# Kernel optimization log

Measured on AMD Instinct MI355X. Metric: run time of the kernel, lower is better.

The kernel has to match this reference:

```python
import jax, jax.numpy as jnp
import numpy as np

VOCAB, X, H, C_CLS = 32000, 300, 512, 5
B, N_LEAVES = 256, 256  # complete binary trees, depth 9, 511 nodes/tree

def setup_inputs() -> dict:
    key = jax.random.key(0)
    ks = jax.random.split(key, 10)
    s = lambda k, shp, fan: jax.random.normal(k, shp, jnp.float32) * (1.0 / np.sqrt(fan))
    return {
        'wordid': jax.random.randint(ks[0], (B, N_LEAVES), 0, VOCAB),
        'emb': jax.random.normal(ks[1], (VOCAB, X), jnp.float32) * 0.1,
        'W_iou_w': s(ks[2], (3 * H, X), X),
        'W_iou_b': jnp.zeros((3 * H,), jnp.float32),
        'U_iou_w': s(ks[3], (3 * H, 2 * H), 2 * H),
        'U_iou_b': jnp.zeros((3 * H,), jnp.float32),
        'U_f_w': s(ks[4], (2 * H, 2 * H), 2 * H),
        'U_f_b': jnp.zeros((2 * H,), jnp.float32),
        'lin_w': s(ks[5], (C_CLS, H), H),
        'lin_b': jnp.zeros((C_CLS,), jnp.float32),
    }

def _cell(iou, c_f):
    i, o, u = jnp.split(iou, 3, axis=-1)
    c = jax.nn.sigmoid(i) * jnp.tanh(u) + c_f
    h = jax.nn.sigmoid(o) * jnp.tanh(c)
    return h, c

def reference(wordid, emb, W_iou_w, W_iou_b, U_iou_w, U_iou_b, U_f_w, U_f_b, lin_w, lin_b):
    b, n = wordid.shape
    # leaves: is_leaf=1 -> iou = W_iou(x), c_f = 0
    x = emb[wordid]                                   # [B, L, X]
    iou = x @ W_iou_w.T + W_iou_b                     # [B, L, 3H]
    h, c = _cell(iou, 0.0)
    hs = [h]
    # internal levels: reduce over exactly 2 children (binary TreeLSTM)
    while h.shape[1] > 1:
        m = h.shape[1] // 2
        h_cat = h.reshape(b, m, 2 * H)                # concat of 2 children
        c_pair = c.reshape(b, m, 2, H)
        f = jax.nn.sigmoid(h_cat @ U_f_w.T + U_f_b).reshape(b, m, 2, H)
        c_f = jnp.sum(f * c_pair, axis=2)             # [B, m, H]
        iou = h_cat @ U_iou_w.T + U_iou_b             # is_leaf=0 branch
        h, c = _cell(iou, c_f)
        hs.append(h)
    h_all = jnp.concatenate(hs, axis=1)               # [B, 2L-1, H], leaves-first topo order
    # dropout is identity at inference
    logits = h_all @ lin_w.T + lin_b                  # [B, 2L-1, num_classes]
    return logits
```

## Files before the change

kernel.cpp:

```cpp
#include <hip/hip_runtime.h>
#include <hip/hip_bf16.h>


typedef __bf16 bf16;
typedef bf16  bf16x8 __attribute__((ext_vector_type(8)));
typedef float f32x4  __attribute__((ext_vector_type(4)));

__device__ __forceinline__ float sigm(float x){ return 1.0f/(1.0f + __expf(-x)); }
__device__ __forceinline__ float tanh_f(float x){ return 1.0f - 2.0f/(__expf(2.0f*x)+1.0f); }

__global__ void cvt_pad_w(const float* __restrict__ src, bf16* __restrict__ dst){
  const int row = blockIdx.x, c = threadIdx.x;
  dst[row*320 + c] = (bf16)(c < 300 ? src[row*300 + c] : 0.f);
}
__global__ void cvt_emb(const float* __restrict__ src, bf16* __restrict__ dst){
  const int row = blockIdx.x, c = threadIdx.x;
  dst[row*320 + c] = (bf16)(c < 300 ? src[(size_t)row*300 + c] : 0.f);
}
__global__ void cvt_u(const float* __restrict__ Uiou, const float* __restrict__ Uf,
                      bf16* __restrict__ dst){
  const int i = blockIdx.x*256 + threadIdx.x;
  if (i < 2560*1024)
    dst[i] = (bf16)(i < 1536*1024 ? Uiou[i] : Uf[i - 1536*1024]);
}

__global__ __launch_bounds__(256, 2)
void leaf128_kernel(const int* __restrict__ wordid, const bf16* __restrict__ embp,
                    const bf16* __restrict__ Wpad, const float* __restrict__ Wb,
                    bf16* __restrict__ hcur, float* __restrict__ ccur)
{
  __shared__ bf16 lsA[128*40];
  __shared__ bf16 lsB[3][64*40];
  const int t = threadIdx.x;
  const int mrow0 = blockIdx.x*128, nblk = blockIdx.y*64;
  const int r = t>>2, kc = (t&3)*8;
  const int lane16 = t&15, quad = (t&63)>>4, w = t>>6;

  f32x4 acc[3][8];
  const f32x4 zero = {0.f,0.f,0.f,0.f};
  #pragma unroll
  for(int o=0;o<3;o++){
    #pragma unroll
    for(int rt=0;rt<8;rt++) acc[o][rt]=zero;
  }

  const int wid0 = wordid[mrow0 + r];
  const int wid1 = wordid[mrow0 + 64 + r];
  const bf16* arow0 = embp + (size_t)wid0*320;
  const bf16* arow1 = embp + (size_t)wid1*320;
  const int col = nblk + r;
  for (int k0=0;k0<320;k0+=32){
    *(bf16x8*)&lsA[r*40+kc]      = *(const bf16x8*)&arow0[k0+kc];
    *(bf16x8*)&lsA[(64+r)*40+kc] = *(const bf16x8*)&arow1[k0+kc];
    #pragma unroll
    for(int g=0;g<3;g++)
      *(bf16x8*)&lsB[g][r*40+kc] = *(const bf16x8*)&Wpad[(size_t)(g*512+col)*320 + k0+kc];
    __syncthreads();
    bf16x8 bfrag[3];
    #pragma unroll
    for(int g=0;g<3;g++) bfrag[g] = *(const bf16x8*)&lsB[g][(w*16+lane16)*40 + quad*8];
    #pragma unroll
    for(int rt=0;rt<8;rt++){
      bf16x8 a = *(const bf16x8*)&lsA[(rt*16+lane16)*40 + quad*8];
      #pragma unroll
      for(int g=0;g<3;g++)
        acc[g][rt] = __builtin_amdgcn_mfma_f32_16x16x32_bf16(a, bfrag[g], acc[g][rt], 0,0,0);
    }
    __syncthreads();
  }
  const int j = nblk + w*16 + lane16;
  const float bi=Wb[j], bo=Wb[512+j], bu=Wb[1024+j];
  #pragma unroll
  for(int rt=0;rt<8;rt++){
    #pragma unroll
    for(int reg=0;reg<4;reg++){
      const int row = mrow0 + rt*16 + quad*4 + reg;
      float iv=acc[0][rt][reg]+bi, ov=acc[1][rt][reg]+bo, uv=acc[2][rt][reg]+bu;
      float c = sigm(iv)*tanh_f(uv);
      float h = sigm(ov)*tanh_f(c);
      ccur[(size_t)row*512 + j] = c;
      hcur[(size_t)row*512 + j] = (bf16)h;
    }
  }
}

__global__ __launch_bounds__(256)
void level_kernel(const bf16* __restrict__ hprev, bf16* __restrict__ hcur,
                  const float* __restrict__ cprev, float* __restrict__ ccur,
                  const bf16* __restrict__ Uall, const float* __restrict__ Uioub,
                  const float* __restrict__ Ufb)
{
  __shared__ bf16 lsA[64*40];
  __shared__ bf16 lsB[5][64*40];
  const int t = threadIdx.x;
  const int mrow0 = blockIdx.x*64, nblk = blockIdx.y*64;
  const int r = t>>2, kc = (t&3)*8;
  const int lane16 = t&15, quad = (t&63)>>4, w = t>>6;

  f32x4 acc[5][4];
  const f32x4 zero = {0.f,0.f,0.f,0.f};
  #pragma unroll
  for(int o=0;o<5;o++){
    #pragma unroll
    for(int rt=0;rt<4;rt++) acc[o][rt]=zero;
  }

  const bf16* arow = hprev + (size_t)(mrow0 + r)*1024;
  const int col = nblk + r;
  for (int k0=0;k0<1024;k0+=32){
    *(bf16x8*)&lsA[r*40+kc] = *(const bf16x8*)&arow[k0+kc];
    #pragma unroll
    for(int g=0;g<5;g++)
      *(bf16x8*)&lsB[g][r*40+kc] = *(const bf16x8*)&Uall[(size_t)(g*512+col)*1024 + k0+kc];
    __syncthreads();
    bf16x8 bfrag[5];
    #pragma unroll
    for(int o=0;o<5;o++) bfrag[o] = *(const bf16x8*)&lsB[o][(w*16+lane16)*40 + quad*8];
    #pragma unroll
    for(int rt=0;rt<4;rt++){
      bf16x8 a = *(const bf16x8*)&lsA[(rt*16+lane16)*40 + quad*8];
      #pragma unroll
      for(int o=0;o<5;o++)
        acc[o][rt] = __builtin_amdgcn_mfma_f32_16x16x32_bf16(a, bfrag[o], acc[o][rt], 0,0,0);
    }
    __syncthreads();
  }
  const int j = nblk + w*16 + lane16;
  const float bi =Uioub[j], bo=Uioub[512+j], bu=Uioub[1024+j];
  const float bfl=Ufb[j],   bfr=Ufb[512+j];
  #pragma unroll
  for(int rt=0;rt<4;rt++){
    #pragma unroll
    for(int reg=0;reg<4;reg++){
      const int row = mrow0 + rt*16 + quad*4 + reg;
      float iv=acc[0][rt][reg]+bi, ov=acc[1][rt][reg]+bo, uv=acc[2][rt][reg]+bu;
      float fl=acc[3][rt][reg]+bfl, fr=acc[4][rt][reg]+bfr;
      float cl = cprev[((size_t)row*2  )*512 + j];
      float cr = cprev[((size_t)row*2+1)*512 + j];
      float cf = sigm(fl)*cl + sigm(fr)*cr;
      float c  = sigm(iv)*tanh_f(uv) + cf;
      float h  = sigm(ov)*tanh_f(c);
      ccur[(size_t)row*512 + j] = c;
      hcur[(size_t)row*512 + j] = (bf16)h;
    }
  }
}

__global__ __launch_bounds__(256, 2)
void level128_kernel(const bf16* __restrict__ hprev, bf16* __restrict__ hcur,
                     const float* __restrict__ cprev, float* __restrict__ ccur,
                     const bf16* __restrict__ Uall, const float* __restrict__ Uioub,
                     const float* __restrict__ Ufb)
{
  __shared__ bf16 lsA[128*40];
  __shared__ bf16 lsB[5][64*40];
  const int t = threadIdx.x;
  const int mrow0 = blockIdx.x*128, nblk = blockIdx.y*64;
  const int r = t>>2, kc = (t&3)*8;
  const int lane16 = t&15, quad = (t&63)>>4, w = t>>6;

  f32x4 acc[5][8];
  const f32x4 zero = {0.f,0.f,0.f,0.f};
  #pragma unroll
  for(int o=0;o<5;o++){
    #pragma unroll
    for(int rt=0;rt<8;rt++) acc[o][rt]=zero;
  }

  const bf16* arow0 = hprev + (size_t)(mrow0 + r)*1024;
  const bf16* arow1 = hprev + (size_t)(mrow0 + 64 + r)*1024;
  const int col = nblk + r;
  for (int k0=0;k0<1024;k0+=32){
    *(bf16x8*)&lsA[r*40+kc]      = *(const bf16x8*)&arow0[k0+kc];
    *(bf16x8*)&lsA[(64+r)*40+kc] = *(const bf16x8*)&arow1[k0+kc];
    #pragma unroll
    for(int g=0;g<5;g++)
      *(bf16x8*)&lsB[g][r*40+kc] = *(const bf16x8*)&Uall[(size_t)(g*512+col)*1024 + k0+kc];
    __syncthreads();
    bf16x8 bfrag[5];
    #pragma unroll
    for(int g=0;g<5;g++) bfrag[g] = *(const bf16x8*)&lsB[g][(w*16+lane16)*40 + quad*8];
    #pragma unroll
    for(int rt=0;rt<8;rt++){
      bf16x8 a = *(const bf16x8*)&lsA[(rt*16+lane16)*40 + quad*8];
      #pragma unroll
      for(int g=0;g<5;g++)
        acc[g][rt] = __builtin_amdgcn_mfma_f32_16x16x32_bf16(a, bfrag[g], acc[g][rt], 0,0,0);
    }
    __syncthreads();
  }
  const int j = nblk + w*16 + lane16;
  const float bi =Uioub[j], bo=Uioub[512+j], bu=Uioub[1024+j];
  const float bfl=Ufb[j],   bfr=Ufb[512+j];
  #pragma unroll
  for(int rt=0;rt<8;rt++){
    #pragma unroll
    for(int reg=0;reg<4;reg++){
      const int row = mrow0 + rt*16 + quad*4 + reg;
      float iv=acc[0][rt][reg]+bi, ov=acc[1][rt][reg]+bo, uv=acc[2][rt][reg]+bu;
      float fl=acc[3][rt][reg]+bfl, fr=acc[4][rt][reg]+bfr;
      float cl = cprev[((size_t)row*2  )*512 + j];
      float cr = cprev[((size_t)row*2+1)*512 + j];
      float cf = sigm(fl)*cl + sigm(fr)*cr;
      float c  = sigm(iv)*tanh_f(uv) + cf;
      float h  = sigm(ov)*tanh_f(c);
      ccur[(size_t)row*512 + j] = c;
      hcur[(size_t)row*512 + j] = (bf16)h;
    }
  }
}

__global__ __launch_bounds__(256)
void logits_kernel(const bf16* __restrict__ h, const float* __restrict__ linw,
                   const float* __restrict__ linb, float* __restrict__ out,
                   int rowbase, int lgm, int mask, int off){
  const int row = blockIdx.x*4 + (threadIdx.x>>6);
  const int l = threadIdx.x & 63;
  bf16x8 hv = *(const bf16x8*)(h + (size_t)row*512 + l*8);
  float hf[8];
  #pragma unroll
  for(int jj=0;jj<8;jj++) hf[jj] = (float)hv[jj];
  float s[5];
  #pragma unroll
  for(int c=0;c<5;c++){
    const f32x4 w0 = *(const f32x4*)(linw + c*512 + l*8);
    const f32x4 w1 = *(const f32x4*)(linw + c*512 + l*8 + 4);
    float a = 0.f;
    #pragma unroll
    for(int jj=0;jj<4;jj++) a += hf[jj]*w0[jj] + hf[4+jj]*w1[jj];
    s[c]=a;
  }
  #pragma unroll
  for(int o=32;o>0;o>>=1){
    #pragma unroll
    for(int c=0;c<5;c++) s[c] += __shfl_down(s[c], o, 64);
  }
  if (l==0){
    const int g = rowbase + row;
    const int node = (g>>lgm)*511 + off + (g&mask);
    #pragma unroll
    for(int c=0;c<5;c++) out[(size_t)node*5+c] = s[c] + linb[c];
  }
}

__global__ void zero_out(float* out, int n){
  int i = blockIdx.x*256 + threadIdx.x;
  if (i < n) out[i] = 0.f;
}

extern "C" void kernel_launch(void* const* d_in, const int* in_sizes, int n_in,
                              void* d_out, int out_size, void* d_ws, size_t ws_size,
                              hipStream_t stream)
{
  const int*   wordid = (const int*)d_in[0];
  const float* emb    = (const float*)d_in[1];
  const float* Wiou   = (const float*)d_in[2];
  const float* Wioub  = (const float*)d_in[3];
  const float* Uiou   = (const float*)d_in[4];
  const float* Uioub  = (const float*)d_in[5];
  const float* Uf     = (const float*)d_in[6];
  const float* Ufb    = (const float*)d_in[7];
  const float* linw   = (const float*)d_in[8];
  const float* linb   = (const float*)d_in[9];
  float* out = (float*)d_out;

  const size_t oWPD  = 0;
  const size_t oUALL = oWPD  + (size_t)1536*320*2;
  const size_t oEMB  = oUALL + (size_t)2560*1024*2;
  const size_t oH1   = oEMB  + (size_t)32000*320*2;
  const size_t oC1   = oH1   + (size_t)32768*512*2;
  const size_t oH0   = oC1   + (size_t)32768*512*4;
  size_t R0 = 0;
  {
    const size_t t2 = oH0 + (size_t)32768*512*(2+4);
    const size_t t4 = oH0 + (size_t)16384*512*(2+4);
    const size_t t8 = oH0 + (size_t) 8192*512*(2+4);
    if      (ws_size >= t2) R0 = 32768;
    else if (ws_size >= t4) R0 = 16384;
    else if (ws_size >= t8) R0 = 8192;
  }
  if (R0 == 0){
    zero_out<<<(out_size+255)/256, 256, 0, stream>>>(out, out_size);
    return;
  }

  char* ws = (char*)d_ws;
  bf16*  Wpad = (bf16*)(ws + oWPD);
  bf16*  Uall = (bf16*)(ws + oUALL);
  bf16*  embp = (bf16*)(ws + oEMB);
  bf16*  h1   = (bf16*)(ws + oH1);
  float* c1   = (float*)(ws + oC1);
  bf16*  h0   = (bf16*)(ws + oH0);
  float* c0   = (float*)(ws + oH0 + R0*1024);

  cvt_pad_w<<<1536, 320, 0, stream>>>(Wiou, Wpad);
  cvt_u<<<(2560*1024+255)/256, 256, 0, stream>>>(Uiou, Uf, Uall);
  cvt_emb<<<32000, 320, 0, stream>>>(emb, embp);

  const int offs[9] = {0,256,384,448,480,496,504,508,510};
  const int nchunk = (int)(65536 / R0);

  for (int ch = 0; ch < nchunk; ch++){
    const int* wid = wordid + (size_t)ch*R0;
    leaf128_kernel<<<dim3((int)(R0/128), 8), 256, 0, stream>>>(wid, embp, Wpad, Wioub,
                                                               h0, c0);
    logits_kernel<<<(int)(R0/4), 256, 0, stream>>>(h0, linw, linb, out,
                                                   (int)(ch*R0), 8, 255, 0);
    bf16*  h1c = h1 + (size_t)ch*(R0/2)*512;
    float* c1c = c1 + (size_t)ch*(R0/2)*512;
    const int orows = (int)(R0/2);
    level128_kernel<<<dim3(orows/128, 8), 256, 0, stream>>>(h0, h1c, c0, c1c,
                                                            Uall, Uioub, Ufb);
  }
  logits_kernel<<<32768/4, 256, 0, stream>>>(h1, linw, linb, out, 0, 7, 127, offs[1]);

  for (int lv = 2; lv <= 8; lv++){
    const int rows = 65536 >> lv;
    const bf16*  hin  = (lv & 1) ? h0 : h1;
    bf16*        hout = (lv & 1) ? h1 : h0;
    const float* cin  = (lv & 1) ? c0 : c1;
    float*       cout = (lv & 1) ? c1 : c0;
    if (rows >= 4096)
      level128_kernel<<<dim3(rows/128, 8), 256, 0, stream>>>(hin, hout, cin, cout,
                                                             Uall, Uioub, Ufb);
    else
      level_kernel<<<dim3(rows/64, 8), 256, 0, stream>>>(hin, hout, cin, cout,
                                                         Uall, Uioub, Ufb);
    logits_kernel<<<rows/4, 256, 0, stream>>>(hout, linw, linb, out,
                                              0, 8-lv, (256>>lv)-1, offs[lv]);
  }
}
```

Before: 871.1 us.

## Load A fragments directly from global and software-prefetch next K tile in level128 kernel

Removes the shared-memory staging of the A (hprev) tile. Each wave loads its MFMA A fragments straight from global memory into registers. Both the A fragments and the next B tile are prefetched one K-step ahead into registers, so global loads overlap with the MFMA work. This adds register pressure (double-buffered A fragments) under launch bounds of 2 blocks, and every wave now redundantly reads the same A rows from global/L2.

Measured after the change: 1.050 ms. 20.6% more time.

```diff
diff --git a/kernel.cpp b/kernel.cpp
--- a/kernel.cpp
+++ b/kernel.cpp
@@ -152,7 +152,6 @@
                      const bf16* __restrict__ Uall, const float* __restrict__ Uioub,
                      const float* __restrict__ Ufb)
 {
-  __shared__ bf16 lsA[128*40];
   __shared__ bf16 lsB[5][64*40];
   const int t = threadIdx.x;
   const int mrow0 = blockIdx.x*128, nblk = blockIdx.y*64;
@@ -167,28 +166,50 @@
     for(int rt=0;rt<8;rt++) acc[o][rt]=zero;
   }
 
-  const bf16* arow0 = hprev + (size_t)(mrow0 + r)*1024;
-  const bf16* arow1 = hprev + (size_t)(mrow0 + 64 + r)*1024;
+  const bf16* gA = hprev + (size_t)(mrow0 + lane16)*1024 + quad*8;
   const int col = nblk + r;
-  for (int k0=0;k0<1024;k0+=32){
-    *(bf16x8*)&lsA[r*40+kc]      = *(const bf16x8*)&arow0[k0+kc];
-    *(bf16x8*)&lsA[(64+r)*40+kc] = *(const bf16x8*)&arow1[k0+kc];
-    #pragma unroll
-    for(int g=0;g<5;g++)
-      *(bf16x8*)&lsB[g][r*40+kc] = *(const bf16x8*)&Uall[(size_t)(g*512+col)*1024 + k0+kc];
-    __syncthreads();
+  const bf16* gBb = Uall + (size_t)col*1024 + kc;
+
+  bf16x8 a_cur[8], a_nxt[8];
+  #pragma unroll
+  for(int rt=0;rt<8;rt++) a_cur[rt] = *(const bf16x8*)(gA + (size_t)rt*16*1024);
+  {
+    bf16x8 sb[5];
+    #pragma unroll
+    for(int g=0;g<5;g++) sb[g] = *(const bf16x8*)(gBb + (size_t)g*512*1024);
+    #pragma unroll
+    for(int g=0;g<5;g++) *(bf16x8*)&lsB[g][r*40+kc] = sb[g];
+  }
+  __syncthreads();
+
+  for (int ks=0; ks<32; ks++){
+    bf16x8 sbn[5];
+    if (ks < 31){
+      const int k1 = (ks+1)*32;
+      #pragma unroll
+      for(int rt=0;rt<8;rt++) a_nxt[rt] = *(const bf16x8*)(gA + (size_t)rt*16*1024 + k1);
+      #pragma unroll
+      for(int g=0;g<5;g++) sbn[g] = *(const bf16x8*)(gBb + (size_t)g*512*1024 + k1);
+    }
     bf16x8 bfrag[5];
     #pragma unroll
     for(int g=0;g<5;g++) bfrag[g] = *(const bf16x8*)&lsB[g][(w*16+lane16)*40 + quad*8];
     #pragma unroll
     for(int rt=0;rt<8;rt++){
-      bf16x8 a = *(const bf16x8*)&lsA[(rt*16+lane16)*40 + quad*8];
       #pragma unroll
       for(int g=0;g<5;g++)
-        acc[g][rt] = __builtin_amdgcn_mfma_f32_16x16x32_bf16(a, bfrag[g], acc[g][rt], 0,0,0);
-    }
-    __syncthreads();
-  }
+        acc[g][rt] = __builtin_amdgcn_mfma_f32_16x16x32_bf16(a_cur[rt], bfrag[g], acc[g][rt], 0,0,0);
+    }
+    if (ks < 31){
+      __syncthreads();
+      #pragma unroll
+      for(int g=0;g<5;g++) *(bf16x8*)&lsB[g][r*40+kc] = sbn[g];
+      __syncthreads();
+      #pragma unroll
+      for(int rt=0;rt<8;rt++) a_cur[rt] = a_nxt[rt];
+    }
+  }
+
   const int j = nblk + w*16 + lane16;
   const float bi =Uioub[j], bo=Uioub[512+j], bu=Uioub[1024+j];
   const float bfl=Ufb[j],   bfr=Ufb[512+j];
```
